# Kernel optimization log

Hardware: AMD Instinct MI355X
Metric: run time of the kernel (lower is better)

The kernel has to match this reference:

```python
import jax, jax.numpy as jnp
import numpy as np

D_IN = 2048
D_OUT = 2048
LN_EPS = 1e-5


def setup_inputs() -> dict:
    key = jax.random.key(0)
    kx, kw, kb = jax.random.split(key, 3)
    x = jax.random.normal(kx, (8, 2048, D_IN), dtype=jnp.float32)
    # LayerNorm affine params (torch defaults: ones / zeros)
    gamma = jnp.ones((D_IN,), dtype=jnp.float32)
    beta = jnp.zeros((D_IN,), dtype=jnp.float32)
    # weight = rand(out,in)*0.001, bias = rand(out)*0.001, alpha = ones(out)
    weight = jax.random.uniform(kw, (D_OUT, D_IN), dtype=jnp.float32) * 0.001
    bias = jax.random.uniform(kb, (D_OUT,), dtype=jnp.float32) * 0.001
    alpha = jnp.ones((D_OUT,), dtype=jnp.float32)
    return {"x": x, "gamma": gamma, "beta": beta, "weight": weight,
            "bias": bias, "alpha": alpha}


def reference(x, gamma, beta, weight, bias, alpha):
    # LayerNorm over last dim (biased variance, eps=1e-5, affine)
    mu = jnp.mean(x, axis=-1, keepdims=True)
    var = jnp.mean(jnp.square(x - mu), axis=-1, keepdims=True)
    xn = (x - mu) * jax.lax.rsqrt(var + LN_EPS) * gamma + beta
    # Binarize activations: hard sign
    a = jnp.sign(xn)
    # Binarize weights: mean-center per output row, clip, sign (STE in fwd == sign)
    centered = weight - jnp.mean(weight, axis=1, keepdims=True)  # [O, I]
    signed_w = jnp.sign(centered)
    # Linear + bias, then per-output-channel alpha scale
    out = jnp.einsum('bsi,oi->bso', a, signed_w) + bias
    return out * alpha
```

## Files before the change

kernel.cpp:

```cpp
#include <hip/hip_runtime.h>

#define DIN 2048
#define WPR 64
#define QPR 32
#define GPR 16
#define RPB 8
#define LN_EPS 1e-5f

#define GLOBAL_AS __attribute__((address_space(1)))
#define LDS_AS    __attribute__((address_space(3)))

typedef unsigned long long u64;
typedef int   i32x4  __attribute__((ext_vector_type(4)));
typedef int   i32x8  __attribute__((ext_vector_type(8)));
typedef float f32x16 __attribute__((ext_vector_type(16)));

__device__ inline float wave_sum(float v) {
    #pragma unroll
    for (int off = 32; off; off >>= 1) v += __shfl_down(v, off, 64);
    return v;
}


__global__ __launch_bounds__(256) void expand_kernel(const float* __restrict__ x,
                                                     const float* __restrict__ gamma,
                                                     const float* __restrict__ beta,
                                                     const float* __restrict__ w,
                                                     char* __restrict__ Aexp,
                                                     char* __restrict__ Bexp,
                                                     int Mblocks) {
    const int t = threadIdx.x;
    const int wid = t >> 6, lane = t & 63;
    __shared__ float red[8];
    __shared__ unsigned stg[RPB * 256];

    const bool isA = (int)blockIdx.x < Mblocks;
    const int r0 = (isA ? blockIdx.x : (blockIdx.x - Mblocks)) * RPB;
    const float* src = isA ? x : w;

    float gg[8], bb[8];
    if (isA) {
        float4 g0 = ((const float4*)gamma)[t * 2];
        float4 g1 = ((const float4*)gamma)[t * 2 + 1];
        float4 b0 = ((const float4*)beta)[t * 2];
        float4 b1 = ((const float4*)beta)[t * 2 + 1];
        gg[0]=g0.x; gg[1]=g0.y; gg[2]=g0.z; gg[3]=g0.w;
        gg[4]=g1.x; gg[5]=g1.y; gg[6]=g1.z; gg[7]=g1.w;
        bb[0]=b0.x; bb[1]=b0.y; bb[2]=b0.z; bb[3]=b0.w;
        bb[4]=b1.x; bb[5]=b1.y; bb[6]=b1.z; bb[7]=b1.w;
    }

    for (int rr = 0; rr < RPB; ++rr) {
        const float* xr = src + (size_t)(r0 + rr) * DIN;
        float4 v0 = ((const float4*)xr)[t * 2];
        float4 v1 = ((const float4*)xr)[t * 2 + 1];
        float vv[8] = {v0.x, v0.y, v0.z, v0.w, v1.x, v1.y, v1.z, v1.w};

        float s = vv[0]+vv[1]+vv[2]+vv[3]+vv[4]+vv[5]+vv[6]+vv[7];
        float ss = 0.f;
        if (isA) {
            #pragma unroll
            for (int j = 0; j < 8; ++j) ss += vv[j] * vv[j];
        }
        float wsum = wave_sum(s);
        float wssum = isA ? wave_sum(ss) : 0.f;
        __syncthreads();
        if (lane == 0) { red[wid] = wsum; red[4 + wid] = wssum; }
        __syncthreads();
        float tot = red[0] + red[1] + red[2] + red[3];
        float mu  = tot * (1.f / DIN);

        unsigned word = 0;
        if (isA) {
            float tots = red[4] + red[5] + red[6] + red[7];
            float var  = tots * (1.f / DIN) - mu * mu;
            float rs   = rsqrtf(var + LN_EPS);
            #pragma unroll
            for (int j = 0; j < 8; ++j) {
                float xn = (vv[j] - mu) * rs * gg[j] + bb[j];
                word |= (xn < 0.f ? 0xAu : 0x2u) << (4 * j);
            }
        } else {
            #pragma unroll
            for (int j = 0; j < 8; ++j)
                word |= ((vv[j] - mu) < 0.f ? 0xAu : 0x2u) << (4 * j);
        }
        stg[rr * 256 + (((t >> 2) ^ rr) << 2) + (t & 3)] = word;
    }
    __syncthreads();

    char* dstbase = isA ? Aexp : Bexp;
    const int bm  = r0 >> 8;
    const int rt  = (r0 >> 5) & 7;
    const int ri0 = r0 & 31;
    #pragma unroll
    for (int i = 0; i < 8; ++i) {
        const int d  = i * 256 + t;
        const int s  = d >> 7;
        const int b  = d & 127;
        const int kt = b >> 6, hb = (b >> 5) & 1, ri = (b >> 2) & 7, e4 = b & 3;
        const size_t doff = (((size_t)(bm * 16 + s)) * 8 + rt) * 2048 + kt * 1024 +
                            (ri0 + ri + 32 * hb) * 16 + e4 * 4;
        const int g = s * 4 + kt * 2 + hb;
        unsigned v = stg[ri * 256 + ((g ^ ri) << 2) + e4];
        *(unsigned*)(dstbase + doff) = v;
    }
}

__global__ __launch_bounds__(512, 2) void fp4gemm_kernel(const char* __restrict__ Aexp,
                                                         const char* __restrict__ Bexp,
                                                         const float* __restrict__ bias,
                                                         const float* __restrict__ alpha,
                                                         float* __restrict__ out,
                                                         int ldc) {
    __shared__ char As[2][16384];
    __shared__ char Bs[2][16384];
    const int t = threadIdx.x;
    const int wid = t >> 6, lane = t & 63;
    const int bn = blockIdx.x & 7;
    const int bm = blockIdx.x >> 3;
    const int wr = wid >> 2;
    const int wc = wid & 3;

    const char* gA = Aexp + (size_t)bm * 16 * 16384;
    const char* gB = Bexp + (size_t)bn * 16 * 16384;

#define STAGE(BUF, S)                                                           \
    {                                                                           \
        _Pragma("unroll")                                                       \
        for (int i2 = 0; i2 < 2; ++i2) {                                        \
            const int ch = i2 * 8 + wid;                                        \
            __builtin_amdgcn_global_load_lds(                                   \
                (const GLOBAL_AS unsigned*)(gA + (size_t)(S) * 16384 + ch * 1024 + lane * 16), \
                (LDS_AS unsigned*)(&As[BUF][ch * 1024]), 16, 0, 0);             \
            __builtin_amdgcn_global_load_lds(                                   \
                (const GLOBAL_AS unsigned*)(gB + (size_t)(S) * 16384 + ch * 1024 + lane * 16), \
                (LDS_AS unsigned*)(&Bs[BUF][ch * 1024]), 16, 0, 0);             \
        }                                                                       \
    }

    f32x16 acc[4][2];
    #pragma unroll
    for (int i = 0; i < 4; ++i)
        #pragma unroll
        for (int j = 0; j < 2; ++j)
            #pragma unroll
            for (int e = 0; e < 16; ++e) acc[i][j][e] = 0.f;

    STAGE(0, 0)
    STAGE(1, 1)
    asm volatile("s_waitcnt vmcnt(4)" ::: "memory");
    __builtin_amdgcn_s_barrier();
    asm volatile("" ::: "memory");

    #pragma unroll 1
    for (int s = 0; s < 16; ++s) {
        const int c = s & 1;
        #pragma unroll
        for (int kt = 0; kt < 2; ++kt) {
            i32x8 a[4], b[2];
            #pragma unroll
            for (int i = 0; i < 4; ++i) {
                i32x4 v = *(const i32x4*)&As[c][(wr * 4 + i) * 2048 + kt * 1024 + lane * 16];
                a[i][0]=v[0]; a[i][1]=v[1]; a[i][2]=v[2]; a[i][3]=v[3];
                a[i][4]=v[0]; a[i][5]=v[1]; a[i][6]=v[2]; a[i][7]=v[3];
            }
            #pragma unroll
            for (int j = 0; j < 2; ++j) {
                i32x4 v = *(const i32x4*)&Bs[c][(wc * 2 + j) * 2048 + kt * 1024 + lane * 16];
                b[j][0]=v[0]; b[j][1]=v[1]; b[j][2]=v[2]; b[j][3]=v[3];
                b[j][4]=v[0]; b[j][5]=v[1]; b[j][6]=v[2]; b[j][7]=v[3];
            }
            __builtin_amdgcn_s_setprio(1);
            #pragma unroll
            for (int i = 0; i < 4; ++i)
                #pragma unroll
                for (int j = 0; j < 2; ++j)
                    acc[i][j] = __builtin_amdgcn_mfma_scale_f32_32x32x64_f8f6f4(
                        a[i], b[j], acc[i][j], 4, 4,
                        0, 0x7F7F7F7F, 0, 0x7F7F7F7F);
            __builtin_amdgcn_s_setprio(0);
        }
        if (s == 15) break;
        asm volatile("s_waitcnt vmcnt(0)" ::: "memory");
        __builtin_amdgcn_s_barrier();
        asm volatile("" ::: "memory");
        if (s < 14) STAGE(c, s + 2)
    }
#undef STAGE

    const int cl = lane & 31;
    const int rb = 4 * (lane >> 5);
    #pragma unroll
    for (int i = 0; i < 4; ++i) {
        #pragma unroll
        for (int j = 0; j < 2; ++j) {
            const int col = bn * 256 + (wc * 2 + j) * 32 + cl;
            const float bi = bias[col], al = alpha[col];
            const int row0 = bm * 256 + (wr * 4 + i) * 32 + rb;
            #pragma unroll
            for (int reg = 0; reg < 16; ++reg) {
                const int row = row0 + (reg & 3) + 8 * (reg >> 2);
                out[(size_t)row * ldc + col] = (acc[i][j][reg] + bi) * al;
            }
        }
    }
}

__global__ __launch_bounds__(256) void w_pack_kernel(const float* __restrict__ w,
                                                     unsigned* __restrict__ wpk) {
    const int row = blockIdx.x;
    const int t = threadIdx.x;
    const float* wr = w + (size_t)row * DIN;
    float4 v0 = ((const float4*)wr)[t * 2];
    float4 v1 = ((const float4*)wr)[t * 2 + 1];
    float s = v0.x + v0.y + v0.z + v0.w + v1.x + v1.y + v1.z + v1.w;

    __shared__ float red[4];
    float wsum = wave_sum(s);
    int wid = t >> 6, lane = t & 63;
    if (lane == 0) red[wid] = wsum;
    __syncthreads();
    float mu = (red[0] + red[1] + red[2] + red[3]) * (1.f / DIN);

    float vv[8] = {v0.x, v0.y, v0.z, v0.w, v1.x, v1.y, v1.z, v1.w};
    unsigned byte = 0;
    #pragma unroll
    for (int j = 0; j < 8; ++j)
        byte |= ((vv[j] - mu) < 0.f ? 1u : 0u) << j;

    __shared__ unsigned char bytes[256];
    bytes[t] = (unsigned char)byte;
    __syncthreads();
    if (t < 64) {
        unsigned wd = (unsigned)bytes[t * 4] | ((unsigned)bytes[t * 4 + 1] << 8) |
                      ((unsigned)bytes[t * 4 + 2] << 16) | ((unsigned)bytes[t * 4 + 3] << 24);
        wpk[(size_t)row * WPR + t] = wd;
    }
}

__global__ __launch_bounds__(256) void ln_pack_kernel(const float* __restrict__ x,
                                                      const float* __restrict__ gamma,
                                                      const float* __restrict__ beta,
                                                      unsigned* __restrict__ apk) {
    const int row = blockIdx.x;
    const int t = threadIdx.x;
    const float* xr = x + (size_t)row * DIN;
    float4 v0 = ((const float4*)xr)[t * 2];
    float4 v1 = ((const float4*)xr)[t * 2 + 1];
    float s  = v0.x + v0.y + v0.z + v0.w + v1.x + v1.y + v1.z + v1.w;
    float ss = v0.x * v0.x + v0.y * v0.y + v0.z * v0.z + v0.w * v0.w +
               v1.x * v1.x + v1.y * v1.y + v1.z * v1.z + v1.w * v1.w;

    __shared__ float red[8];
    float wsum = wave_sum(s), wssum = wave_sum(ss);
    int wid = t >> 6, lane = t & 63;
    if (lane == 0) { red[wid] = wsum; red[4 + wid] = wssum; }
    __syncthreads();
    float tot  = red[0] + red[1] + red[2] + red[3];
    float tots = red[4] + red[5] + red[6] + red[7];
    float mu  = tot * (1.f / DIN);
    float var = tots * (1.f / DIN) - mu * mu;
    float rs  = rsqrtf(var + LN_EPS);

    float4 g0 = ((const float4*)gamma)[t * 2];
    float4 g1 = ((const float4*)gamma)[t * 2 + 1];
    float4 b0 = ((const float4*)beta)[t * 2];
    float4 b1 = ((const float4*)beta)[t * 2 + 1];
    float vv[8] = {v0.x, v0.y, v0.z, v0.w, v1.x, v1.y, v1.z, v1.w};
    float gg[8] = {g0.x, g0.y, g0.z, g0.w, g1.x, g1.y, g1.z, g1.w};
    float bb[8] = {b0.x, b0.y, b0.z, b0.w, b1.x, b1.y, b1.z, b1.w};
    unsigned byte = 0;
    #pragma unroll
    for (int j = 0; j < 8; ++j) {
        float xn = (vv[j] - mu) * rs * gg[j] + bb[j];
        byte |= (xn < 0.f ? 1u : 0u) << j;
    }

    __shared__ unsigned char bytes[256];
    bytes[t] = (unsigned char)byte;
    __syncthreads();
    if (t < 64) {
        unsigned wd = (unsigned)bytes[t * 4] | ((unsigned)bytes[t * 4 + 1] << 8) |
                      ((unsigned)bytes[t * 4 + 2] << 16) | ((unsigned)bytes[t * 4 + 3] << 24);
        apk[(size_t)row * WPR + t] = wd;
    }
}

__global__ __launch_bounds__(256) void bingemm_kernel(const u64* __restrict__ A,
                                                      const u64* __restrict__ B,
                                                      const float* __restrict__ bias,
                                                      const float* __restrict__ alpha,
                                                      float* __restrict__ out) {
    __shared__ u64 S[2 * 128 * QPR];
    uint4* Sg = (uint4*)S;
    const int t = threadIdx.x;
    const int bn = blockIdx.x, bm = blockIdx.y;

    const uint4* Ag = (const uint4*)(A + (size_t)bm * 128 * QPR);
    #pragma unroll
    for (int i = 0; i < 8; ++i) {
        int id = t + i * 256;
        int row = id >> 4, g = id & 15;
        Sg[(row << 4) + (g ^ (row & 15))] = Ag[id];
    }
    const uint4* Bg = (const uint4*)(B + (size_t)bn * 128 * QPR);
    #pragma unroll
    for (int i = 0; i < 8; ++i) {
        int id = t + i * 256;
        int row = id >> 4, g = id & 15;
        Sg[2048 + (row << 4) + (g ^ (row & 15))] = Bg[id];
    }
    __syncthreads();

    const int tr = t >> 4;
    const int tc = t & 15;
    const ulonglong2* Sq = (const ulonglong2*)S;
    const int abase = tr * GPR;
    const int bbase = 2048 + tc * GPR;

    int acc[8][8] = {};
    u64 a0[8][2], b0[8][2], a1[8][2], b1[8][2];

#define LOADK(KK, AR, BR)                                            \
    {                                                                \
        const int ka = abase + ((KK) ^ tr);                          \
        const int kb = bbase + ((KK) ^ tc);                          \
        _Pragma("unroll")                                            \
        for (int r = 0; r < 8; ++r) {                                \
            ulonglong2 v = Sq[ka + r * 256];                         \
            AR[r][0] = v.x; AR[r][1] = v.y;                          \
        }                                                            \
        _Pragma("unroll")                                            \
        for (int c2 = 0; c2 < 8; ++c2) {                             \
            ulonglong2 v = Sq[kb + c2 * 256];                        \
            BR[c2][0] = v.x; BR[c2][1] = v.y;                        \
        }                                                            \
    }

#define COMPK(AR, BR)                                                \
    {                                                                \
        _Pragma("unroll")                                            \
        for (int r = 0; r < 8; ++r) {                                \
            _Pragma("unroll")                                        \
            for (int c2 = 0; c2 < 8; ++c2) {                         \
                acc[r][c2] += __popcll(AR[r][0] ^ BR[c2][0]);        \
                acc[r][c2] += __popcll(AR[r][1] ^ BR[c2][1]);        \
            }                                                        \
        }                                                            \
    }

    LOADK(0, a0, b0);
    #pragma unroll 1
    for (int kk = 0; kk < 14; kk += 2) {
        LOADK(kk + 1, a1, b1);
        COMPK(a0, b0);
        LOADK(kk + 2, a0, b0);
        COMPK(a1, b1);
    }
    LOADK(15, a1, b1);
    COMPK(a0, b0);
    COMPK(a1, b1);
#undef LOADK
#undef COMPK

    float bi[8], al[8];
    #pragma unroll
    for (int c2 = 0; c2 < 8; ++c2) {
        int col = bn * 128 + tc + 16 * c2;
        bi[c2] = bias[col];
        al[c2] = alpha[col];
    }
    #pragma unroll
    for (int r = 0; r < 8; ++r) {
        const size_t row = (size_t)bm * 128 + tr + 16 * r;
        float* op = out + row * 2048 + bn * 128 + tc;
        #pragma unroll
        for (int c2 = 0; c2 < 8; ++c2)
            op[16 * c2] = ((float)(DIN - 2 * acc[r][c2]) + bi[c2]) * al[c2];
    }
}

extern "C" void kernel_launch(void* const* d_in, const int* in_sizes, int n_in,
                              void* d_out, int out_size, void* d_ws, size_t ws_size,
                              hipStream_t stream) {
    const float* x     = (const float*)d_in[0];
    const float* gamma = (const float*)d_in[1];
    const float* beta  = (const float*)d_in[2];
    const float* w     = (const float*)d_in[3];
    const float* bias  = (const float*)d_in[4];
    const float* alpha = (const float*)d_in[5];
    float* out = (float*)d_out;

    const int M = in_sizes[0] / DIN;
    const int N = in_sizes[3] / DIN;

    const size_t needA = (size_t)M * (DIN / 2);
    const size_t needB = (size_t)N * (DIN / 2);

    if (ws_size >= needA + needB && (M % 256) == 0 && (N % 256) == 0) {
        char* Aexp = (char*)d_ws;
        char* Bexp = (char*)d_ws + needA;
        expand_kernel<<<(M + N) / RPB, 256, 0, stream>>>(x, gamma, beta, w,
                                                         Aexp, Bexp, M / RPB);
        dim3 grid((N / 256) * (M / 256));
        fp4gemm_kernel<<<grid, 512, 0, stream>>>(Aexp, Bexp, bias, alpha, out, N);
    } else {
        unsigned* apk = (unsigned*)d_ws;
        unsigned* wpk = (unsigned*)((char*)d_ws + (size_t)M * WPR * 4);
        w_pack_kernel<<<N, 256, 0, stream>>>(w, wpk);
        ln_pack_kernel<<<M, 256, 0, stream>>>(x, gamma, beta, apk);
        dim3 grid(N / 128, M / 128);
        bingemm_kernel<<<grid, 256, 0, stream>>>((const u64*)apk, (const u64*)wpk,
                                                 bias, alpha, out);
    }
}
```

Measured before the change: 90.34 us.

## Triple-buffer GEMM LDS stages and give each wave whole rows in expand kernel

```diff
diff --git a/kernel.cpp b/kernel.cpp
--- a/kernel.cpp
+++ b/kernel.cpp
@@ -18,6 +18,12 @@
 __device__ inline float wave_sum(float v) {
     #pragma unroll
     for (int off = 32; off; off >>= 1) v += __shfl_down(v, off, 64);
+    return v;
+}
+
+__device__ inline float wave_sum_all(float v) {
+    #pragma unroll
+    for (int off = 1; off < 64; off <<= 1) v += __shfl_xor(v, off, 64);
     return v;
 }
 
@@ -30,62 +36,68 @@
                                                      char* __restrict__ Bexp,
                                                      int Mblocks) {
     const int t = threadIdx.x;
-    const int wid = t >> 6, lane = t & 63;
-    __shared__ float red[8];
+    const int wv = t >> 6, lane = t & 63;
     __shared__ unsigned stg[RPB * 256];
 
     const bool isA = (int)blockIdx.x < Mblocks;
-    const int r0 = (isA ? blockIdx.x : (blockIdx.x - Mblocks)) * RPB;
+    const int r0 = (isA ? (int)blockIdx.x : ((int)blockIdx.x - Mblocks)) * RPB;
     const float* src = isA ? x : w;
 
-    float gg[8], bb[8];
+    float gg[32], bb[32];
     if (isA) {
-        float4 g0 = ((const float4*)gamma)[t * 2];
-        float4 g1 = ((const float4*)gamma)[t * 2 + 1];
-        float4 b0 = ((const float4*)beta)[t * 2];
-        float4 b1 = ((const float4*)beta)[t * 2 + 1];
-        gg[0]=g0.x; gg[1]=g0.y; gg[2]=g0.z; gg[3]=g0.w;
-        gg[4]=g1.x; gg[5]=g1.y; gg[6]=g1.z; gg[7]=g1.w;
-        bb[0]=b0.x; bb[1]=b0.y; bb[2]=b0.z; bb[3]=b0.w;
-        bb[4]=b1.x; bb[5]=b1.y; bb[6]=b1.z; bb[7]=b1.w;
-    }
-
-    for (int rr = 0; rr < RPB; ++rr) {
-        const float* xr = src + (size_t)(r0 + rr) * DIN;
-        float4 v0 = ((const float4*)xr)[t * 2];
-        float4 v1 = ((const float4*)xr)[t * 2 + 1];
-        float vv[8] = {v0.x, v0.y, v0.z, v0.w, v1.x, v1.y, v1.z, v1.w};
-
-        float s = vv[0]+vv[1]+vv[2]+vv[3]+vv[4]+vv[5]+vv[6]+vv[7];
-        float ss = 0.f;
+        #pragma unroll
+        for (int q = 0; q < 8; ++q) {
+            float4 g = ((const float4*)gamma)[lane * 8 + q];
+            float4 b = ((const float4*)beta)[lane * 8 + q];
+            gg[4*q+0]=g.x; gg[4*q+1]=g.y; gg[4*q+2]=g.z; gg[4*q+3]=g.w;
+            bb[4*q+0]=b.x; bb[4*q+1]=b.y; bb[4*q+2]=b.z; bb[4*q+3]=b.w;
+        }
+    }
+
+    #pragma unroll
+    for (int rw = 0; rw < 2; ++rw) {
+        const int rr = wv * 2 + rw;
+        const float* xr = src + (size_t)(r0 + rr) * DIN + lane * 32;
+        float vv[32];
+        #pragma unroll
+        for (int q = 0; q < 8; ++q) {
+            float4 v = ((const float4*)xr)[q];
+            vv[4*q+0]=v.x; vv[4*q+1]=v.y; vv[4*q+2]=v.z; vv[4*q+3]=v.w;
+        }
+        float s = 0.f;
+        #pragma unroll
+        for (int j = 0; j < 32; ++j) s += vv[j];
+        float mu, rs = 0.f;
         if (isA) {
-            #pragma unroll
-            for (int j = 0; j < 8; ++j) ss += vv[j] * vv[j];
-        }
-        float wsum = wave_sum(s);
-        float wssum = isA ? wave_sum(ss) : 0.f;
-        __syncthreads();
-        if (lane == 0) { red[wid] = wsum; red[4 + wid] = wssum; }
-        __syncthreads();
-        float tot = red[0] + red[1] + red[2] + red[3];
-        float mu  = tot * (1.f / DIN);
-
-        unsigned word = 0;
-        if (isA) {
-            float tots = red[4] + red[5] + red[6] + red[7];
-            float var  = tots * (1.f / DIN) - mu * mu;
-            float rs   = rsqrtf(var + LN_EPS);
+            float ss = 0.f;
+            #pragma unroll
+            for (int j = 0; j < 32; ++j) ss += vv[j] * vv[j];
+            s  = wave_sum_all(s);
+            ss = wave_sum_all(ss);
+            mu = s * (1.f / DIN);
+            float var = ss * (1.f / DIN) - mu * mu;
+            rs = rsqrtf(var + LN_EPS);
+        } else {
+            s = wave_sum_all(s);
+            mu = s * (1.f / DIN);
+        }
+
+        unsigned wds[4];
+        #pragma unroll
+        for (int e = 0; e < 4; ++e) {
+            unsigned word = 0;
             #pragma unroll
             for (int j = 0; j < 8; ++j) {
-                float xn = (vv[j] - mu) * rs * gg[j] + bb[j];
-                word |= (xn < 0.f ? 0xAu : 0x2u) << (4 * j);
+                float xv = vv[8 * e + j];
+                bool neg;
+                if (isA) neg = ((xv - mu) * rs * gg[8 * e + j] + bb[8 * e + j]) < 0.f;
+                else     neg = (xv - mu) < 0.f;
+                word |= (neg ? 0xAu : 0x2u) << (4 * j);
             }
-        } else {
-            #pragma unroll
-            for (int j = 0; j < 8; ++j)
-                word |= ((vv[j] - mu) < 0.f ? 0xAu : 0x2u) << (4 * j);
-        }
-        stg[rr * 256 + (((t >> 2) ^ rr) << 2) + (t & 3)] = word;
+            wds[e] = word;
+        }
+        *(uint4*)&stg[rr * 256 + ((lane ^ rr) << 2)] =
+            make_uint4(wds[0], wds[1], wds[2], wds[3]);
     }
     __syncthreads();
 
@@ -96,12 +108,12 @@
     #pragma unroll
     for (int i = 0; i < 8; ++i) {
         const int d  = i * 256 + t;
-        const int s  = d >> 7;
+        const int sc = d >> 7;
         const int b  = d & 127;
         const int kt = b >> 6, hb = (b >> 5) & 1, ri = (b >> 2) & 7, e4 = b & 3;
-        const size_t doff = (((size_t)(bm * 16 + s)) * 8 + rt) * 2048 + kt * 1024 +
+        const size_t doff = (((size_t)(bm * 16 + sc)) * 8 + rt) * 2048 + kt * 1024 +
                             (ri0 + ri + 32 * hb) * 16 + e4 * 4;
-        const int g = s * 4 + kt * 2 + hb;
+        const int g = sc * 4 + kt * 2 + hb;
         unsigned v = stg[ri * 256 + ((g ^ ri) << 2) + e4];
         *(unsigned*)(dstbase + doff) = v;
     }
@@ -113,8 +125,8 @@
                                                          const float* __restrict__ alpha,
                                                          float* __restrict__ out,
                                                          int ldc) {
-    __shared__ char As[2][16384];
-    __shared__ char Bs[2][16384];
+    __shared__ char As[3][16384];
+    __shared__ char Bs[3][16384];
     const int t = threadIdx.x;
     const int wid = t >> 6, lane = t & 63;
     const int bn = blockIdx.x & 7;
@@ -149,13 +161,14 @@
 
     STAGE(0, 0)
     STAGE(1, 1)
-    asm volatile("s_waitcnt vmcnt(4)" ::: "memory");
+    STAGE(2, 2)
+    asm volatile("s_waitcnt vmcnt(8)" ::: "memory");
     __builtin_amdgcn_s_barrier();
     asm volatile("" ::: "memory");
 
+    int c = 0;
     #pragma unroll 1
     for (int s = 0; s < 16; ++s) {
-        const int c = s & 1;
         #pragma unroll
         for (int kt = 0; kt < 2; ++kt) {
             i32x8 a[4], b[2];
@@ -182,10 +195,12 @@
             __builtin_amdgcn_s_setprio(0);
         }
         if (s == 15) break;
-        asm volatile("s_waitcnt vmcnt(0)" ::: "memory");
+        if (s <= 13) { asm volatile("s_waitcnt vmcnt(4)" ::: "memory"); }
+        else         { asm volatile("s_waitcnt vmcnt(0)" ::: "memory"); }
         __builtin_amdgcn_s_barrier();
         asm volatile("" ::: "memory");
-        if (s < 14) STAGE(c, s + 2)
+        if (s <= 12) STAGE(c, s + 3)
+        c = (c == 2) ? 0 : c + 1;
     }
 #undef STAGE
 
```

Result: slower. 99.94 us (+10.6%).
